# Kernel tuning notes

Measured on AMD Instinct MI355X. Metric: run time of the kernel, lower is better.

## Reference

```python
import jax, jax.numpy as jnp
import numpy as np

B, S, H, L = 64, 2048, 1024, 15


def setup_inputs() -> dict:
    key = jax.random.key(0)
    ks = jax.random.split(key, 16)
    x = jax.random.normal(ks[0], (B, S, H), dtype=jnp.float32)
    # valid spans: start in [1, S-40), length in [1, 32)
    s1 = jax.random.randint(ks[1], (B,), 1, S - 40)
    l1 = jax.random.randint(ks[2], (B,), 1, 32)
    s2 = jax.random.randint(ks[3], (B,), 1, S - 40)
    l2 = jax.random.randint(ks[4], (B,), 1, 32)
    entity_idx = jnp.stack([s1, s1 + l1, s2, s2 + l2], axis=1).astype(jnp.int32)
    sc = 1.0 / np.sqrt(H)
    W_cls = jax.random.normal(ks[5], (H, H), jnp.float32) * sc
    b_cls = jnp.zeros((H,), jnp.float32)
    W_e1 = jax.random.normal(ks[6], (H, H), jnp.float32) * sc
    b_e1 = jnp.zeros((H,), jnp.float32)
    W_e2 = jax.random.normal(ks[7], (H, H), jnp.float32) * sc
    b_e2 = jnp.zeros((H,), jnp.float32)
    W1 = jax.random.normal(ks[8], (3 * H, H), jnp.float32) * (1.0 / np.sqrt(3 * H))
    b1 = jnp.zeros((H,), jnp.float32)
    W2 = jax.random.normal(ks[9], (H, H), jnp.float32) * sc
    b2 = jnp.zeros((H,), jnp.float32)
    Wout = jax.random.normal(ks[10], (H, L), jnp.float32) * sc
    bout = jnp.zeros((L,), jnp.float32)
    return {"x": x, "entity_idx": entity_idx, "W_cls": W_cls, "b_cls": b_cls,
            "W_e1": W_e1, "b_e1": b_e1, "W_e2": W_e2, "b_e2": b_e2,
            "W1": W1, "b1": b1, "W2": W2, "b2": b2, "Wout": Wout, "bout": bout}


def _span_mean(x, start, end):
    # x: [B,S,H]; start,end: [B] int -> masked mean over [start,end)
    pos = jnp.arange(x.shape[1])[None, :]  # [1,S]
    mask = ((pos >= start[:, None]) & (pos < end[:, None])).astype(x.dtype)  # [B,S]
    cnt = jnp.maximum(mask.sum(axis=1, keepdims=True), 1.0)  # [B,1]
    return jnp.einsum('bs,bsh->bh', mask, x) / cnt


def reference(x, entity_idx, W_cls, b_cls, W_e1, b_e1, W_e2, b_e2,
              W1, b1, W2, b2, Wout, bout):
    subj = _span_mean(x, entity_idx[:, 0], entity_idx[:, 1])  # [B,H]
    obj = _span_mean(x, entity_idx[:, 2], entity_idx[:, 3])   # [B,H]
    x0 = jnp.tanh(x[:, 0, :]) @ W_cls + b_cls
    e1 = jnp.tanh(subj) @ W_e1 + b_e1
    e2 = jnp.tanh(obj) @ W_e2 + b_e2
    h = jnp.concatenate([x0, e1, e2], axis=1)  # [B,3H]
    h = h @ W1 + b1           # dropout is identity at eval
    h = h @ W2 + b2
    out = h @ Wout + bout     # [B,num_labels]
    return out
```

## Files before the change

kernel.cpp:

```cpp
#include <hip/hip_runtime.h>
#include <math.h>

#define BB 64
#define SS 2048
#define HH 1024
#define LL 15

__global__ void span_tanh_kernel(const float* __restrict__ x,
                                 const int* __restrict__ eidx,
                                 float* __restrict__ t_cat,
                                 float* __restrict__ h_cat,
                                 float* __restrict__ h1,
                                 float* __restrict__ h2) {
  int b = blockIdx.x;
  int hc = blockIdx.y;
  int tid = threadIdx.x;
  int h = hc * 256 + tid;

  {
    float* z = h_cat + (size_t)b * 3 * HH + hc * 768;
    for (int i = tid; i < 768; i += 256) z[i] = 0.f;
    h1[(size_t)b * HH + hc * 256 + tid] = 0.f;
    h2[(size_t)b * HH + hc * 256 + tid] = 0.f;
  }

  int s1 = eidx[b * 4 + 0], e1 = eidx[b * 4 + 1];
  int s2 = eidx[b * 4 + 2], e2 = eidx[b * 4 + 3];
  float c1 = (float)max(e1 - s1, 1);
  float c2 = (float)max(e2 - s2, 1);
  const float* xb = x + (size_t)b * SS * HH;
  float* tb = t_cat + (size_t)b * 3 * HH;

  float v0 = xb[h];
  float a1 = 0.f, a2 = 0.f;
  for (int s = s1; s < e1; ++s) a1 += xb[(size_t)s * HH + h];
  for (int s = s2; s < e2; ++s) a2 += xb[(size_t)s * HH + h];
  tb[h]          = tanhf(v0);
  tb[HH + h]     = tanhf(a1 / c1);
  tb[2 * HH + h] = tanhf(a2 / c2);
}

#define LSTR 68
__device__ __forceinline__ void gemm_tile_body(
    const float* __restrict__ A, int lda,
    const float* __restrict__ W, int ldw,
    const float* __restrict__ bias,
    float* __restrict__ C, int ldc,
    int k0, int kend, int j0, bool addBias) {
  __shared__ float As[32 * LSTR];
  __shared__ float Ws[32 * LSTR];
  int tid = threadIdx.x;
  int tx = tid & 15, ty = tid >> 4;

  float4 aReg[2], wReg[2];
  int aRow[2], aKq[2], wRow[2], wCq[2];
#pragma unroll
  for (int i = 0; i < 2; ++i) {
    int idx = tid + i * 256;
    aRow[i] = idx & 63; aKq[i] = idx >> 6;
    wRow[i] = idx >> 4; wCq[i] = idx & 15;
  }

  auto loadRegs = [&](int kb) {
#pragma unroll
    for (int i = 0; i < 2; ++i) {
      aReg[i] = *(const float4*)&A[(size_t)aRow[i] * lda + kb + 4 * aKq[i]];
      wReg[i] = *(const float4*)&W[(size_t)(kb + wRow[i]) * ldw + j0 + 4 * wCq[i]];
    }
  };

  float acc[4][4] = {{0.f}};
  loadRegs(k0);
  for (int kb = k0; kb < kend; kb += 32) {
#pragma unroll
    for (int i = 0; i < 2; ++i) {
      float av[4] = {aReg[i].x, aReg[i].y, aReg[i].z, aReg[i].w};
#pragma unroll
      for (int j = 0; j < 4; ++j) As[(4 * aKq[i] + j) * LSTR + aRow[i]] = av[j];
      *(float4*)&Ws[wRow[i] * LSTR + 4 * wCq[i]] = wReg[i];
    }
    __syncthreads();
    if (kb + 32 < kend) loadRegs(kb + 32);
#pragma unroll
    for (int kk = 0; kk < 32; ++kk) {
      float4 a4 = *(const float4*)&As[kk * LSTR + ty * 4];
      float4 w4 = *(const float4*)&Ws[kk * LSTR + tx * 4];
      float a[4] = {a4.x, a4.y, a4.z, a4.w};
      float w[4] = {w4.x, w4.y, w4.z, w4.w};
#pragma unroll
      for (int i = 0; i < 4; ++i)
#pragma unroll
        for (int j = 0; j < 4; ++j) acc[i][j] += a[i] * w[j];
    }
    __syncthreads();
  }
#pragma unroll
  for (int i = 0; i < 4; ++i) {
    int r = ty * 4 + i;
#pragma unroll
    for (int j = 0; j < 4; ++j) {
      int c = j0 + tx * 4 + j;
      float v = acc[i][j];
      if (addBias) v += bias[c];
      atomicAdd(&C[(size_t)r * ldc + c], v);
    }
  }
}

__global__ void gemm_bd_kernel(const float* __restrict__ t_cat,
                               const float* __restrict__ Wc, const float* __restrict__ bc,
                               const float* __restrict__ We1, const float* __restrict__ be1,
                               const float* __restrict__ We2, const float* __restrict__ be2,
                               float* __restrict__ h_cat, int Kchunk) {
  int z = blockIdx.z;
  const float* W = (z == 0) ? Wc : ((z == 1) ? We1 : We2);
  const float* bias = (z == 0) ? bc : ((z == 1) ? be1 : be2);
  const float* A = t_cat + z * HH;
  float* C = h_cat + z * HH;
  int k0 = blockIdx.y * Kchunk;
  gemm_tile_body(A, 3 * HH, W, HH, bias, C, 3 * HH,
                 k0, k0 + Kchunk, blockIdx.x * 64, blockIdx.y == 0);
}

__global__ void gemm_kernel(const float* __restrict__ A, int lda,
                            const float* __restrict__ W, int ldw,
                            const float* __restrict__ bias,
                            float* __restrict__ C, int ldc, int Kchunk) {
  int k0 = blockIdx.y * Kchunk;
  gemm_tile_body(A, lda, W, ldw, bias, C, ldc,
                 k0, k0 + Kchunk, blockIdx.x * 64, blockIdx.y == 0);
}

__global__ void out_kernel(const float* __restrict__ h2,
                           const float* __restrict__ Wout,
                           const float* __restrict__ bout,
                           float* __restrict__ out) {
  int tid = threadIdx.x;
  int lane = tid & 63;
  int idx = blockIdx.x * 4 + (tid >> 6);
  int b = idx / LL, l = idx % LL;
  const float* h = h2 + (size_t)b * HH;
  float acc = 0.f;
#pragma unroll
  for (int w = 0; w < 4; ++w) {
    int k0 = (w * 64 + lane) * 4;
    float4 h4 = *(const float4*)&h[k0];
    acc += h4.x * Wout[(size_t)(k0 + 0) * LL + l];
    acc += h4.y * Wout[(size_t)(k0 + 1) * LL + l];
    acc += h4.z * Wout[(size_t)(k0 + 2) * LL + l];
    acc += h4.w * Wout[(size_t)(k0 + 3) * LL + l];
  }
#pragma unroll
  for (int off = 32; off > 0; off >>= 1) acc += __shfl_down(acc, off, 64);
  if (lane == 0) out[idx] = acc + bout[l];
}

extern "C" void kernel_launch(void* const* d_in, const int* in_sizes, int n_in,
                              void* d_out, int out_size, void* d_ws, size_t ws_size,
                              hipStream_t stream) {
  const float* x     = (const float*)d_in[0];
  const int*   eidx  = (const int*)d_in[1];
  const float* W_cls = (const float*)d_in[2];
  const float* b_cls = (const float*)d_in[3];
  const float* W_e1  = (const float*)d_in[4];
  const float* b_e1  = (const float*)d_in[5];
  const float* W_e2  = (const float*)d_in[6];
  const float* b_e2  = (const float*)d_in[7];
  const float* W1    = (const float*)d_in[8];
  const float* b1    = (const float*)d_in[9];
  const float* W2    = (const float*)d_in[10];
  const float* b2    = (const float*)d_in[11];
  const float* Wout  = (const float*)d_in[12];
  const float* bout  = (const float*)d_in[13];
  float* out = (float*)d_out;

  float* ws    = (float*)d_ws;
  float* t_cat = ws;
  float* h_cat = t_cat + BB * 3 * HH;
  float* h1    = h_cat + BB * 3 * HH;
  float* h2    = h1 + BB * HH;

  span_tanh_kernel<<<dim3(BB, 4), 256, 0, stream>>>(x, eidx, t_cat, h_cat, h1, h2);

  gemm_bd_kernel<<<dim3(16, 4, 3), 256, 0, stream>>>(
      t_cat, W_cls, b_cls, W_e1, b_e1, W_e2, b_e2, h_cat, 256);

  gemm_kernel<<<dim3(16, 12, 1), 256, 0, stream>>>(h_cat, 3 * HH, W1, HH, b1, h1, HH, 256);

  gemm_kernel<<<dim3(16, 8, 1), 256, 0, stream>>>(h1, HH, W2, HH, b2, h2, HH, 128);

  out_kernel<<<dim3(240), 256, 0, stream>>>(h2, Wout, bout, out);
}
```

Measured before the change: 726.4 us.

## Fuse all stages into one cooperative persistent kernel with grid syncs

Replaces the five separate launches (span mean/tanh, three GEMM stages, output projection) with one cooperative kernel of 256 blocks. Stages are separated by grid.sync() and the work is remapped to block indices. The split-K partitioning also changes: W1 now uses 16 K-slices of 192 instead of 12 of 256, and W2 uses 16 of 64 instead of 8 of 128. This removes launch gaps between small kernels, at the cost of grid-wide barriers, idle blocks in some stages, and more atomics from the finer split-K.

```diff
diff --git a/kernel.cpp b/kernel.cpp
--- a/kernel.cpp
+++ b/kernel.cpp
@@ -1,54 +1,22 @@
 #include <hip/hip_runtime.h>
+#include <hip/hip_cooperative_groups.h>
 #include <math.h>
+
+namespace cg = cooperative_groups;
 
 #define BB 64
 #define SS 2048
 #define HH 1024
 #define LL 15
-
-__global__ void span_tanh_kernel(const float* __restrict__ x,
-                                 const int* __restrict__ eidx,
-                                 float* __restrict__ t_cat,
-                                 float* __restrict__ h_cat,
-                                 float* __restrict__ h1,
-                                 float* __restrict__ h2) {
-  int b = blockIdx.x;
-  int hc = blockIdx.y;
-  int tid = threadIdx.x;
-  int h = hc * 256 + tid;
-
-  {
-    float* z = h_cat + (size_t)b * 3 * HH + hc * 768;
-    for (int i = tid; i < 768; i += 256) z[i] = 0.f;
-    h1[(size_t)b * HH + hc * 256 + tid] = 0.f;
-    h2[(size_t)b * HH + hc * 256 + tid] = 0.f;
-  }
-
-  int s1 = eidx[b * 4 + 0], e1 = eidx[b * 4 + 1];
-  int s2 = eidx[b * 4 + 2], e2 = eidx[b * 4 + 3];
-  float c1 = (float)max(e1 - s1, 1);
-  float c2 = (float)max(e2 - s2, 1);
-  const float* xb = x + (size_t)b * SS * HH;
-  float* tb = t_cat + (size_t)b * 3 * HH;
-
-  float v0 = xb[h];
-  float a1 = 0.f, a2 = 0.f;
-  for (int s = s1; s < e1; ++s) a1 += xb[(size_t)s * HH + h];
-  for (int s = s2; s < e2; ++s) a2 += xb[(size_t)s * HH + h];
-  tb[h]          = tanhf(v0);
-  tb[HH + h]     = tanhf(a1 / c1);
-  tb[2 * HH + h] = tanhf(a2 / c2);
-}
-
 #define LSTR 68
+
 __device__ __forceinline__ void gemm_tile_body(
+    float* __restrict__ As, float* __restrict__ Ws,
     const float* __restrict__ A, int lda,
     const float* __restrict__ W, int ldw,
     const float* __restrict__ bias,
     float* __restrict__ C, int ldc,
     int k0, int kend, int j0, bool addBias) {
-  __shared__ float As[32 * LSTR];
-  __shared__ float Ws[32 * LSTR];
   int tid = threadIdx.x;
   int tx = tid & 15, ty = tid >> 4;
 
@@ -107,52 +75,96 @@
   }
 }
 
-__global__ void gemm_bd_kernel(const float* __restrict__ t_cat,
-                               const float* __restrict__ Wc, const float* __restrict__ bc,
-                               const float* __restrict__ We1, const float* __restrict__ be1,
-                               const float* __restrict__ We2, const float* __restrict__ be2,
-                               float* __restrict__ h_cat, int Kchunk) {
-  int z = blockIdx.z;
-  const float* W = (z == 0) ? Wc : ((z == 1) ? We1 : We2);
-  const float* bias = (z == 0) ? bc : ((z == 1) ? be1 : be2);
-  const float* A = t_cat + z * HH;
-  float* C = h_cat + z * HH;
-  int k0 = blockIdx.y * Kchunk;
-  gemm_tile_body(A, 3 * HH, W, HH, bias, C, 3 * HH,
-                 k0, k0 + Kchunk, blockIdx.x * 64, blockIdx.y == 0);
-}
-
-__global__ void gemm_kernel(const float* __restrict__ A, int lda,
-                            const float* __restrict__ W, int ldw,
-                            const float* __restrict__ bias,
-                            float* __restrict__ C, int ldc, int Kchunk) {
-  int k0 = blockIdx.y * Kchunk;
-  gemm_tile_body(A, lda, W, ldw, bias, C, ldc,
-                 k0, k0 + Kchunk, blockIdx.x * 64, blockIdx.y == 0);
-}
-
-__global__ void out_kernel(const float* __restrict__ h2,
-                           const float* __restrict__ Wout,
-                           const float* __restrict__ bout,
-                           float* __restrict__ out) {
+__global__ void __launch_bounds__(256, 1) fused_kernel(
+    const float* __restrict__ x, const int* __restrict__ eidx,
+    const float* __restrict__ W_cls, const float* __restrict__ b_cls,
+    const float* __restrict__ W_e1, const float* __restrict__ b_e1,
+    const float* __restrict__ W_e2, const float* __restrict__ b_e2,
+    const float* __restrict__ W1, const float* __restrict__ b1,
+    const float* __restrict__ W2, const float* __restrict__ b2,
+    const float* __restrict__ Wout, const float* __restrict__ bout,
+    float* __restrict__ t_cat, float* __restrict__ h_cat,
+    float* __restrict__ h1, float* __restrict__ h2,
+    float* __restrict__ out) {
+  cg::grid_group grid = cg::this_grid();
+  __shared__ float smem[2 * 32 * LSTR];
+  float* As = smem;
+  float* Ws = smem + 32 * LSTR;
+  int r = blockIdx.x;
   int tid = threadIdx.x;
-  int lane = tid & 63;
-  int idx = blockIdx.x * 4 + (tid >> 6);
-  int b = idx / LL, l = idx % LL;
-  const float* h = h2 + (size_t)b * HH;
-  float acc = 0.f;
-#pragma unroll
-  for (int w = 0; w < 4; ++w) {
-    int k0 = (w * 64 + lane) * 4;
-    float4 h4 = *(const float4*)&h[k0];
-    acc += h4.x * Wout[(size_t)(k0 + 0) * LL + l];
-    acc += h4.y * Wout[(size_t)(k0 + 1) * LL + l];
-    acc += h4.z * Wout[(size_t)(k0 + 2) * LL + l];
-    acc += h4.w * Wout[(size_t)(k0 + 3) * LL + l];
-  }
-#pragma unroll
-  for (int off = 32; off > 0; off >>= 1) acc += __shfl_down(acc, off, 64);
-  if (lane == 0) out[idx] = acc + bout[l];
+
+  {
+    int b = r >> 2, hc = r & 3;
+    int h = hc * 256 + tid;
+    float* z = h_cat + (size_t)b * 3 * HH + hc * 768;
+    for (int i = tid; i < 768; i += 256) z[i] = 0.f;
+    h1[(size_t)b * HH + h] = 0.f;
+    h2[(size_t)b * HH + h] = 0.f;
+
+    int s1 = eidx[b * 4 + 0], e1 = eidx[b * 4 + 1];
+    int s2 = eidx[b * 4 + 2], e2 = eidx[b * 4 + 3];
+    float c1 = (float)max(e1 - s1, 1);
+    float c2 = (float)max(e2 - s2, 1);
+    const float* xb = x + (size_t)b * SS * HH;
+    float* tb = t_cat + (size_t)b * 3 * HH;
+    float v0 = xb[h];
+    float a1 = 0.f, a2 = 0.f;
+    for (int s = s1; s < e1; ++s) a1 += xb[(size_t)s * HH + h];
+    for (int s = s2; s < e2; ++s) a2 += xb[(size_t)s * HH + h];
+    tb[h]          = tanhf(v0);
+    tb[HH + h]     = tanhf(a1 / c1);
+    tb[2 * HH + h] = tanhf(a2 / c2);
+  }
+  grid.sync();
+
+  if (r < 192) {
+    int zb = r >> 6;
+    int rem = r & 63;
+    int jt = rem & 15;
+    int ks = rem >> 4;
+    const float* W = (zb == 0) ? W_cls : ((zb == 1) ? W_e1 : W_e2);
+    const float* bias = (zb == 0) ? b_cls : ((zb == 1) ? b_e1 : b_e2);
+    gemm_tile_body(As, Ws, t_cat + zb * HH, 3 * HH, W, HH, bias,
+                   h_cat + zb * HH, 3 * HH,
+                   ks * 256, ks * 256 + 256, jt * 64, ks == 0);
+  }
+  grid.sync();
+
+  {
+    int jt = r & 15, ks = r >> 4;
+    gemm_tile_body(As, Ws, h_cat, 3 * HH, W1, HH, b1, h1, HH,
+                   ks * 192, ks * 192 + 192, jt * 64, ks == 0);
+  }
+  grid.sync();
+
+  {
+    int jt = r & 15, ks = r >> 4;
+    gemm_tile_body(As, Ws, h1, HH, W2, HH, b2, h2, HH,
+                   ks * 64, ks * 64 + 64, jt * 64, ks == 0);
+  }
+  grid.sync();
+
+  {
+    int lane = tid & 63;
+    int idx = r * 4 + (tid >> 6);
+    if (idx < BB * LL) {
+      int b = idx / LL, l = idx % LL;
+      const float* h = h2 + (size_t)b * HH;
+      float acc = 0.f;
+#pragma unroll
+      for (int w = 0; w < 4; ++w) {
+        int k0 = (w * 64 + lane) * 4;
+        float4 h4 = *(const float4*)&h[k0];
+        acc += h4.x * Wout[(size_t)(k0 + 0) * LL + l];
+        acc += h4.y * Wout[(size_t)(k0 + 1) * LL + l];
+        acc += h4.z * Wout[(size_t)(k0 + 2) * LL + l];
+        acc += h4.w * Wout[(size_t)(k0 + 3) * LL + l];
+      }
+#pragma unroll
+      for (int off = 32; off > 0; off >>= 1) acc += __shfl_down(acc, off, 64);
+      if (lane == 0) out[idx] = acc + bout[l];
+    }
+  }
 }
 
 extern "C" void kernel_launch(void* const* d_in, const int* in_sizes, int n_in,
@@ -180,14 +192,13 @@
   float* h1    = h_cat + BB * 3 * HH;
   float* h2    = h1 + BB * HH;
 
-  span_tanh_kernel<<<dim3(BB, 4), 256, 0, stream>>>(x, eidx, t_cat, h_cat, h1, h2);
-
-  gemm_bd_kernel<<<dim3(16, 4, 3), 256, 0, stream>>>(
-      t_cat, W_cls, b_cls, W_e1, b_e1, W_e2, b_e2, h_cat, 256);
-
-  gemm_kernel<<<dim3(16, 12, 1), 256, 0, stream>>>(h_cat, 3 * HH, W1, HH, b1, h1, HH, 256);
-
-  gemm_kernel<<<dim3(16, 8, 1), 256, 0, stream>>>(h1, HH, W2, HH, b2, h2, HH, 128);
-
-  out_kernel<<<dim3(240), 256, 0, stream>>>(h2, Wout, bout, out);
+  void* args[] = {
+    (void*)&x, (void*)&eidx,
+    (void*)&W_cls, (void*)&b_cls, (void*)&W_e1, (void*)&b_e1,
+    (void*)&W_e2, (void*)&b_e2, (void*)&W1, (void*)&b1,
+    (void*)&W2, (void*)&b2, (void*)&Wout, (void*)&bout,
+    (void*)&t_cat, (void*)&h_cat, (void*)&h1, (void*)&h2, (void*)&out
+  };
+  hipLaunchCooperativeKernel((const void*)fused_kernel,
+                             dim3(256), dim3(256), args, 0, stream);
 }
```

Measured after the change: 830.7 us. 1.14x slower.
